# Optimization experiments

Hardware: AMD Instinct MI355X
Metric: run time of the kernel (lower is better)

## Reference

```python
import jax, jax.numpy as jnp
import numpy as np
from jax import lax

B, T, I, H = 64, 2048, 64, 256


def setup_inputs() -> dict:
    key = jax.random.key(0)
    ks = jax.random.split(key, 7)
    s = 1.0 / np.sqrt(H)  # PyTorch LSTM/Linear init scale
    x = jax.random.normal(ks[0], (B, T, I), dtype=jnp.float32)
    W_ih = jax.random.uniform(ks[1], (4 * H, I), minval=-s, maxval=s, dtype=jnp.float32)
    W_hh = jax.random.uniform(ks[2], (4 * H, H), minval=-s, maxval=s, dtype=jnp.float32)
    b_ih = jax.random.uniform(ks[3], (4 * H,), minval=-s, maxval=s, dtype=jnp.float32)
    b_hh = jax.random.uniform(ks[4], (4 * H,), minval=-s, maxval=s, dtype=jnp.float32)
    W_o = jax.random.uniform(ks[5], (1, H), minval=-s, maxval=s, dtype=jnp.float32)
    b_o = jax.random.uniform(ks[6], (1,), minval=-s, maxval=s, dtype=jnp.float32)
    return {"x": x, "W_ih": W_ih, "W_hh": W_hh, "b_ih": b_ih, "b_hh": b_hh, "W_o": W_o, "b_o": b_o}


def _lstm(x, W_ih, W_hh, b_ih, b_hh):
    # x: [B, T, I]. PyTorch gate order: i, f, g, o.
    Bn, Tn, _ = x.shape
    Hn = W_hh.shape[1]
    # Precompute input contribution for all timesteps (one big GEMM).
    gx = jnp.einsum('bti,gi->btg', x, W_ih) + b_ih + b_hh  # [B, T, 4H]

    def step(carry, gxt):
        h, c = carry
        gates = gxt + h @ W_hh.T  # [B, 4H]
        i, f, g, o = jnp.split(gates, 4, axis=-1)
        c = jax.nn.sigmoid(f) * c + jax.nn.sigmoid(i) * jnp.tanh(g)
        h = jax.nn.sigmoid(o) * jnp.tanh(c)
        return (h, c), h

    h0 = jnp.zeros((Bn, Hn), x.dtype)
    (_, _), hs = lax.scan(step, (h0, h0), jnp.swapaxes(gx, 0, 1))  # hs: [T, B, H]
    return jnp.swapaxes(hs, 0, 1)  # [B, T, H]


def reference(x, W_ih, W_hh, b_ih, b_hh, W_o, b_o):
    hs = _lstm(x, W_ih, W_hh, b_ih, b_hh)          # [B, T, H]
    return hs @ W_o.T + b_o                         # [B, T, 1]
```

## Files before the change

### kernel.cpp

```cpp
#include <hip/hip_runtime.h>
#include <hip/hip_fp16.h>

#define B_  64
#define T_  2048
#define I_  64
#define H_  256
#define G4_ 1024

typedef _Float16 h2v __attribute__((ext_vector_type(2)));

__device__ __forceinline__ float fdot2(uint32_t a, uint32_t b, float c) {
#if __has_builtin(__builtin_amdgcn_fdot2)
    return __builtin_amdgcn_fdot2(__builtin_bit_cast(h2v, a), __builtin_bit_cast(h2v, b), c, false);
#else
    h2v ha = __builtin_bit_cast(h2v, a), hb = __builtin_bit_cast(h2v, b);
    return c + (float)ha.x * (float)hb.x + (float)ha.y * (float)hb.y;
#endif
}

__device__ __forceinline__ ushort f2h(float v) {
    return __builtin_bit_cast(ushort, (_Float16)v);
}
__device__ __forceinline__ float h2f(ushort v) {
    return (float)__builtin_bit_cast(_Float16, v);
}

__global__ void repack_kernel(const float* __restrict__ Whh, ushort* __restrict__ wpk) {
    int o  = blockIdx.x * 256 + threadIdx.x;
    int j  = o & 7;
    int h  = (o >> 3) & 255;
    int kc = (o >> 11) & 31;
    int g  = o >> 16;
    float v = Whh[(g * 256 + h) * 256 + kc * 8 + j];
    wpk[o] = f2h(v);
}

__global__ __launch_bounds__(256) void gx_kernel(
    const float* __restrict__ x, const float* __restrict__ Wih,
    const float* __restrict__ bih, const float* __restrict__ bhh,
    ushort* __restrict__ gx2, int t0, int TCc) {

    __shared__ float xs[32][64];
    const int bt0 = blockIdx.x * 32;
    const int gq  = blockIdx.y;
    const int row = gq * 256 + threadIdx.x;

    for (int i = threadIdx.x; i < 512; i += 256) {
        int r  = i >> 4, c4 = i & 15;
        int bt = bt0 + r;
        int b  = bt / TCc;
        int tl = bt - b * TCc;
        *(float4*)(&xs[r][c4 * 4]) =
            *(const float4*)(&x[(((size_t)b * T_) + t0 + tl) * I_ + c4 * 4]);
    }
    __syncthreads();

    float w[64];
#pragma unroll
    for (int k = 0; k < 64; ++k) w[k] = Wih[row * I_ + k];
    const float bias = bih[row] + bhh[row];

    for (int i = 0; i < 32; ++i) {
        float acc = bias;
#pragma unroll
        for (int k4 = 0; k4 < 16; ++k4) {
            float4 xq = *(const float4*)(&xs[i][k4 * 4]);
            acc = fmaf(w[k4 * 4 + 0], xq.x, acc);
            acc = fmaf(w[k4 * 4 + 1], xq.y, acc);
            acc = fmaf(w[k4 * 4 + 2], xq.z, acc);
            acc = fmaf(w[k4 * 4 + 3], xq.w, acc);
        }
        gx2[((size_t)(bt0 + i) * 256 + threadIdx.x) * 4 + gq] = f2h(acc);
    }
}

__global__ __launch_bounds__(512, 1)
void lstm_kernel(
    const ushort* __restrict__ wpk, const ushort* __restrict__ gx2,
    ushort* __restrict__ hbuf,
    float* __restrict__ state,
    int TCc, int first) {

    __shared__ __align__(16) ushort wg4[14 * 2 * 256 * 8];
    __shared__ __align__(16) ushort hs[256];
    __shared__ __align__(16) float pex[256][4];

    const int tid   = threadIdx.x;
    const int hd    = tid & 255;
    const int q     = tid >> 8;
    const int kbase = q << 4;
    const int b     = blockIdx.x;
    const bool q0   = (q == 0);

    uint32_t wi[64], wf[64], wg[64];
#pragma unroll
    for (int k = 0; k < 16; ++k) {
        uint4 v = *(const uint4*)(wpk + (size_t)(0 * 32 + kbase + k) * 2048 + hd * 8);
        wi[k * 4 + 0] = v.x; wi[k * 4 + 1] = v.y; wi[k * 4 + 2] = v.z; wi[k * 4 + 3] = v.w;
    }
#pragma unroll
    for (int k = 0; k < 16; ++k) {
        uint4 v = *(const uint4*)(wpk + (size_t)(1 * 32 + kbase + k) * 2048 + hd * 8);
        wf[k * 4 + 0] = v.x; wf[k * 4 + 1] = v.y; wf[k * 4 + 2] = v.z; wf[k * 4 + 3] = v.w;
    }
#pragma unroll
    for (int k = 0; k < 16; ++k) {
        uint4 v = *(const uint4*)(wpk + (size_t)(2 * 32 + kbase + k) * 2048 + hd * 8);
        wg[k * 4 + 0] = v.x; wg[k * 4 + 1] = v.y; wg[k * 4 + 2] = v.z; wg[k * 4 + 3] = v.w;
    }
#pragma unroll
    for (int k = 0; k < 14; ++k) {
        uint4 v = *(const uint4*)(wpk + (size_t)(3 * 32 + kbase + k) * 2048 + hd * 8);
        *(uint4*)(wg4 + ((k * 2 + q) * 256 + hd) * 8) = v;
    }
    uint32_t wo_r[8];
#pragma unroll
    for (int k = 0; k < 2; ++k) {
        uint4 v = *(const uint4*)(wpk + (size_t)(3 * 32 + kbase + 14 + k) * 2048 + hd * 8);
        wo_r[k * 4 + 0] = v.x; wo_r[k * 4 + 1] = v.y; wo_r[k * 4 + 2] = v.z; wo_r[k * 4 + 3] = v.w;
    }

    float c = 0.f, h = 0.f;
    if (q0) {
        if (!first) {
            c = state[b * H_ + hd];
            h = state[B_ * H_ + b * H_ + hd];
        }
        hs[hd] = f2h(h);
    }
    __syncthreads();

    const ushort* gxb = gx2 + (size_t)b * TCc * G4_;
    ushort* hb = hbuf + (size_t)b * TCc * H_;

    ushort4 cg;
    if (q0) cg = *(const ushort4*)(gxb + (size_t)0 * G4_ + hd * 4);

    for (int tl = 0; tl < TCc; ++tl) {
        ushort4 ng;
        if (q0) {
            const int tn = (tl + 1 < TCc) ? tl + 1 : tl;
            ng = *(const ushort4*)(gxb + (size_t)tn * G4_ + hd * 4);
        }

        float ai = 0.f, af = 0.f, agv = 0.f, ao = 0.f;

#pragma unroll
        for (int k = 0; k < 14; ++k) {
            const int kc = kbase + k;
            uint4 hq = *(const uint4*)(hs + kc * 8);
            uint4 wo = *(const uint4*)(wg4 + ((k * 2 + q) * 256 + hd) * 8);
            ai  = fdot2(wi[k * 4 + 0], hq.x, ai);
            ai  = fdot2(wi[k * 4 + 1], hq.y, ai);
            ai  = fdot2(wi[k * 4 + 2], hq.z, ai);
            ai  = fdot2(wi[k * 4 + 3], hq.w, ai);
            af  = fdot2(wf[k * 4 + 0], hq.x, af);
            af  = fdot2(wf[k * 4 + 1], hq.y, af);
            af  = fdot2(wf[k * 4 + 2], hq.z, af);
            af  = fdot2(wf[k * 4 + 3], hq.w, af);
            agv = fdot2(wg[k * 4 + 0], hq.x, agv);
            agv = fdot2(wg[k * 4 + 1], hq.y, agv);
            agv = fdot2(wg[k * 4 + 2], hq.z, agv);
            agv = fdot2(wg[k * 4 + 3], hq.w, agv);
            ao  = fdot2(wo.x, hq.x, ao);
            ao  = fdot2(wo.y, hq.y, ao);
            ao  = fdot2(wo.z, hq.z, ao);
            ao  = fdot2(wo.w, hq.w, ao);
        }
#pragma unroll
        for (int k = 14; k < 16; ++k) {
            const int kc = kbase + k;
            const int r  = (k - 14) * 4;
            uint4 hq = *(const uint4*)(hs + kc * 8);
            ai  = fdot2(wi[k * 4 + 0], hq.x, ai);
            ai  = fdot2(wi[k * 4 + 1], hq.y, ai);
            ai  = fdot2(wi[k * 4 + 2], hq.z, ai);
            ai  = fdot2(wi[k * 4 + 3], hq.w, ai);
            af  = fdot2(wf[k * 4 + 0], hq.x, af);
            af  = fdot2(wf[k * 4 + 1], hq.y, af);
            af  = fdot2(wf[k * 4 + 2], hq.z, af);
            af  = fdot2(wf[k * 4 + 3], hq.w, af);
            agv = fdot2(wg[k * 4 + 0], hq.x, agv);
            agv = fdot2(wg[k * 4 + 1], hq.y, agv);
            agv = fdot2(wg[k * 4 + 2], hq.z, agv);
            agv = fdot2(wg[k * 4 + 3], hq.w, agv);
            ao  = fdot2(wo_r[r + 0], hq.x, ao);
            ao  = fdot2(wo_r[r + 1], hq.y, ao);
            ao  = fdot2(wo_r[r + 2], hq.z, ao);
            ao  = fdot2(wo_r[r + 3], hq.w, ao);
        }

        if (!q0) {
            float4 p; p.x = ai; p.y = af; p.z = agv; p.w = ao;
            *(float4*)(&pex[hd][0]) = p;
        }
        __syncthreads();

        if (q0) {
            float4 px = *(const float4*)(&pex[hd][0]);
            ai += px.x; af += px.y; agv += px.z; ao += px.w;

            ai += h2f(cg.x); af += h2f(cg.y); agv += h2f(cg.z); ao += h2f(cg.w);

            float si = __builtin_amdgcn_rcpf(1.f + __expf(-ai));
            float sf = __builtin_amdgcn_rcpf(1.f + __expf(-af));
            float so = __builtin_amdgcn_rcpf(1.f + __expf(-ao));
            float eg = __expf(2.f * agv);
            float tg = (eg - 1.f) * __builtin_amdgcn_rcpf(eg + 1.f);
            c = sf * c + si * tg;
            float ec = __expf(2.f * c);
            float tc = (ec - 1.f) * __builtin_amdgcn_rcpf(ec + 1.f);
            h = so * tc;

            ushort hh = f2h(h);
            hs[hd] = hh;
            hb[(size_t)tl * H_ + hd] = hh;
            cg = ng;
        }
        __syncthreads();
    }

    if (q0) {
        state[b * H_ + hd]           = c;
        state[B_ * H_ + b * H_ + hd] = h;
    }
}

__global__ __launch_bounds__(256) void proj_kernel(
    const ushort* __restrict__ hbuf, const float* __restrict__ Wo,
    const float* __restrict__ bo, float* __restrict__ out, int t0, int TCc) {

    const int lane = threadIdx.x & 63;
    const int wid  = blockIdx.x * 4 + (threadIdx.x >> 6);
    const int nw   = gridDim.x * 4;
    const int rows = B_ * TCc;

    float4 w = *(const float4*)(Wo + lane * 4);
    const float bov = bo[0];

    for (int r = wid; r < rows; r += nw) {
        const ushort* hp = hbuf + (size_t)r * H_ + lane * 4;
        ushort4 u = *(const ushort4*)hp;
        float p = h2f(u.x) * w.x + h2f(u.y) * w.y + h2f(u.z) * w.z + h2f(u.w) * w.w;
#pragma unroll
        for (int m = 1; m < 64; m <<= 1) p += __shfl_xor(p, m, 64);
        if (lane == 0) {
            int b  = r / TCc;
            int tl = r - b * TCc;
            out[(size_t)b * T_ + t0 + tl] = p + bov;
        }
    }
}

extern "C" void kernel_launch(void* const* d_in, const int* in_sizes, int n_in,
                              void* d_out, int out_size, void* d_ws, size_t ws_size,
                              hipStream_t stream) {
    const float* x   = (const float*)d_in[0];
    const float* Wih = (const float*)d_in[1];
    const float* Whh = (const float*)d_in[2];
    const float* bih = (const float*)d_in[3];
    const float* bhh = (const float*)d_in[4];
    const float* Wo  = (const float*)d_in[5];
    const float* bo  = (const float*)d_in[6];
    float* out = (float*)d_out;

    char* ws = (char*)d_ws;
    ushort* wpk   = (ushort*)ws;
    float*  state = (float*)(ws + 512 * 1024);
    char*   dyn   = ws + 640 * 1024;

    size_t avail = (ws_size > 640 * 1024) ? ws_size - 640 * 1024 : 0;
    long long tcmax = (long long)(avail / ((size_t)B_ * (G4_ + H_) * 2));
    int TC = (tcmax > 512) ? 512 : (int)tcmax;
    TC &= ~63;
    if (TC < 64) TC = 64;

    repack_kernel<<<1024, 256, 0, stream>>>(Whh, wpk);

    for (int t0 = 0; t0 < T_; t0 += TC) {
        int TCc = (T_ - t0 < TC) ? (T_ - t0) : TC;
        ushort* gxb  = (ushort*)dyn;
        ushort* hbuf = (ushort*)(dyn + (size_t)B_ * TCc * G4_ * 2);
        dim3 g1((B_ * TCc) / 32, 4);
        gx_kernel<<<g1, 256, 0, stream>>>(x, Wih, bih, bhh, gxb, t0, TCc);
        lstm_kernel<<<B_, 512, 0, stream>>>(wpk, gxb, hbuf, state, TCc, t0 == 0 ? 1 : 0);
        proj_kernel<<<256, 256, 0, stream>>>(hbuf, Wo, bo, out, t0, TCc);
    }
    (void)in_sizes; (void)n_in; (void)out_size;
}
```

Measured before the change: 3.327 ms.

## Use fp16 dot2 in input GEMM and defer projection to one full-sequence launch

The input-projection kernel now packs x and W_ih into fp16 pairs and accumulates with fdot2, halving LDS footprint and the number of multiply instructions. The hidden-state buffer is enlarged to hold the whole sequence, so the output projection runs once after all chunks instead of once per chunk, removing per-chunk launches. The extra fp16 rounding of x and W_ih adds precision loss, and the larger workspace requirement can shrink the chunk size when workspace is limited.

```diff
diff --git a/kernel.cpp b/kernel.cpp
--- a/kernel.cpp
+++ b/kernel.cpp
@@ -40,7 +40,7 @@
     const float* __restrict__ bih, const float* __restrict__ bhh,
     ushort* __restrict__ gx2, int t0, int TCc) {
 
-    __shared__ float xs[32][64];
+    __shared__ uint32_t xsp[32][32];
     const int bt0 = blockIdx.x * 32;
     const int gq  = blockIdx.y;
     const int row = gq * 256 + threadIdx.x;
@@ -50,25 +50,30 @@
         int bt = bt0 + r;
         int b  = bt / TCc;
         int tl = bt - b * TCc;
-        *(float4*)(&xs[r][c4 * 4]) =
-            *(const float4*)(&x[(((size_t)b * T_) + t0 + tl) * I_ + c4 * 4]);
+        float4 v = *(const float4*)(&x[(((size_t)b * T_) + t0 + tl) * I_ + c4 * 4]);
+        xsp[r][c4 * 2 + 0] = (uint32_t)f2h(v.x) | ((uint32_t)f2h(v.y) << 16);
+        xsp[r][c4 * 2 + 1] = (uint32_t)f2h(v.z) | ((uint32_t)f2h(v.w) << 16);
     }
     __syncthreads();
 
-    float w[64];
-#pragma unroll
-    for (int k = 0; k < 64; ++k) w[k] = Wih[row * I_ + k];
+    uint32_t wp[32];
+#pragma unroll
+    for (int k = 0; k < 32; ++k) {
+        float a = Wih[row * I_ + 2 * k];
+        float b = Wih[row * I_ + 2 * k + 1];
+        wp[k] = (uint32_t)f2h(a) | ((uint32_t)f2h(b) << 16);
+    }
     const float bias = bih[row] + bhh[row];
 
     for (int i = 0; i < 32; ++i) {
         float acc = bias;
 #pragma unroll
-        for (int k4 = 0; k4 < 16; ++k4) {
-            float4 xq = *(const float4*)(&xs[i][k4 * 4]);
-            acc = fmaf(w[k4 * 4 + 0], xq.x, acc);
-            acc = fmaf(w[k4 * 4 + 1], xq.y, acc);
-            acc = fmaf(w[k4 * 4 + 2], xq.z, acc);
-            acc = fmaf(w[k4 * 4 + 3], xq.w, acc);
+        for (int k4 = 0; k4 < 8; ++k4) {
+            uint4 xq = *(const uint4*)(&xsp[i][k4 * 4]);
+            acc = fdot2(wp[k4 * 4 + 0], xq.x, acc);
+            acc = fdot2(wp[k4 * 4 + 1], xq.y, acc);
+            acc = fdot2(wp[k4 * 4 + 2], xq.z, acc);
+            acc = fdot2(wp[k4 * 4 + 3], xq.w, acc);
         }
         gx2[((size_t)(bt0 + i) * 256 + threadIdx.x) * 4 + gq] = f2h(acc);
     }
@@ -79,7 +84,7 @@
     const ushort* __restrict__ wpk, const ushort* __restrict__ gx2,
     ushort* __restrict__ hbuf,
     float* __restrict__ state,
-    int TCc, int first) {
+    int TCc, int t0, int first) {
 
     __shared__ __align__(16) ushort wg4[14 * 2 * 256 * 8];
     __shared__ __align__(16) ushort hs[256];
@@ -131,7 +136,7 @@
     __syncthreads();
 
     const ushort* gxb = gx2 + (size_t)b * TCc * G4_;
-    ushort* hb = hbuf + (size_t)b * TCc * H_;
+    ushort* hb = hbuf + (size_t)b * T_ * H_ + (size_t)t0 * H_;
 
     ushort4 cg;
     if (q0) cg = *(const ushort4*)(gxb + (size_t)0 * G4_ + hd * 4);
@@ -228,12 +233,12 @@
 
 __global__ __launch_bounds__(256) void proj_kernel(
     const ushort* __restrict__ hbuf, const float* __restrict__ Wo,
-    const float* __restrict__ bo, float* __restrict__ out, int t0, int TCc) {
+    const float* __restrict__ bo, float* __restrict__ out) {
 
     const int lane = threadIdx.x & 63;
     const int wid  = blockIdx.x * 4 + (threadIdx.x >> 6);
     const int nw   = gridDim.x * 4;
-    const int rows = B_ * TCc;
+    const int rows = B_ * T_;
 
     float4 w = *(const float4*)(Wo + lane * 4);
     const float bov = bo[0];
@@ -244,11 +249,7 @@
         float p = h2f(u.x) * w.x + h2f(u.y) * w.y + h2f(u.z) * w.z + h2f(u.w) * w.w;
 #pragma unroll
         for (int m = 1; m < 64; m <<= 1) p += __shfl_xor(p, m, 64);
-        if (lane == 0) {
-            int b  = r / TCc;
-            int tl = r - b * TCc;
-            out[(size_t)b * T_ + t0 + tl] = p + bov;
-        }
+        if (lane == 0) out[r] = p + bov;
     }
 }
 
@@ -267,10 +268,13 @@
     char* ws = (char*)d_ws;
     ushort* wpk   = (ushort*)ws;
     float*  state = (float*)(ws + 512 * 1024);
-    char*   dyn   = ws + 640 * 1024;
-
-    size_t avail = (ws_size > 640 * 1024) ? ws_size - 640 * 1024 : 0;
-    long long tcmax = (long long)(avail / ((size_t)B_ * (G4_ + H_) * 2));
+    ushort* hbuf  = (ushort*)(ws + 640 * 1024);
+    const size_t hbuf_bytes = (size_t)B_ * T_ * H_ * 2;
+    char*   dyn   = ws + 640 * 1024 + hbuf_bytes;
+
+    size_t fixed = 640 * 1024 + hbuf_bytes;
+    size_t avail = (ws_size > fixed) ? ws_size - fixed : 0;
+    long long tcmax = (long long)(avail / ((size_t)B_ * G4_ * 2));
     int TC = (tcmax > 512) ? 512 : (int)tcmax;
     TC &= ~63;
     if (TC < 64) TC = 64;
@@ -279,12 +283,11 @@
 
     for (int t0 = 0; t0 < T_; t0 += TC) {
         int TCc = (T_ - t0 < TC) ? (T_ - t0) : TC;
-        ushort* gxb  = (ushort*)dyn;
-        ushort* hbuf = (ushort*)(dyn + (size_t)B_ * TCc * G4_ * 2);
+        ushort* gxb = (ushort*)dyn;
         dim3 g1((B_ * TCc) / 32, 4);
         gx_kernel<<<g1, 256, 0, stream>>>(x, Wih, bih, bhh, gxb, t0, TCc);
-        lstm_kernel<<<B_, 512, 0, stream>>>(wpk, gxb, hbuf, state, TCc, t0 == 0 ? 1 : 0);
-        proj_kernel<<<256, 256, 0, stream>>>(hbuf, Wo, bo, out, t0, TCc);
-    }
+        lstm_kernel<<<B_, 512, 0, stream>>>(wpk, gxb, hbuf, state, TCc, t0, t0 == 0 ? 1 : 0);
+    }
+    proj_kernel<<<512, 256, 0, stream>>>(hbuf, Wo, bo, out);
     (void)in_sizes; (void)n_in; (void)out_size;
 }
```

After: 3.123 ms. -6.1%, faster.
